# Performance work log

Measured on AMD Instinct MI355X. Metric: run time of the kernel, lower is better.

The kernel has to match this reference:

```python
import jax, jax.numpy as jnp
import numpy as np

V, F, H, R = 10000, 768, 768, 49
B, T = 128, 32


def setup_inputs() -> dict:
    key = jax.random.key(0)
    ks = jax.random.split(key, 12)
    s = lambda *sh: 1.0 / np.sqrt(sh[-1])
    return {
        "features": jax.random.normal(ks[0], (B, R, F), jnp.float32),
        "captions": jax.random.randint(ks[1], (B, T), 0, V),
        "emb_W": jax.random.normal(ks[2], (V, H), jnp.float32),
        "attn_W": jax.random.normal(ks[3], (H, F + H), jnp.float32) * s(H, F + H),
        "attn_b": jnp.zeros((H,), jnp.float32),
        "attnv_W": jax.random.normal(ks[4], (1, H), jnp.float32) * s(1, H),
        "attnv_b": jnp.zeros((1,), jnp.float32),
        "W_ih": jax.random.normal(ks[5], (4 * H, H + F), jnp.float32) * s(1, H),
        "W_hh": jax.random.normal(ks[6], (4 * H, H), jnp.float32) * s(1, H),
        "b_ih": jnp.zeros((4 * H,), jnp.float32),
        "b_hh": jnp.zeros((4 * H,), jnp.float32),
        "fc_W": jax.random.normal(ks[7], (V, H), jnp.float32) * s(V, H),
        "fc_b": jnp.zeros((V,), jnp.float32),
    }


def reference(features, captions, emb_W, attn_W, attn_b, attnv_W, attnv_b,
              W_ih, W_hh, b_ih, b_hh, fc_W, fc_b):
    # initial hidden state (hidden_state=None branch)
    h0 = jnp.tanh(features.mean(axis=1))           # [B,H]
    c0 = jnp.zeros_like(h0)                        # [B,H]
    emb = emb_W[captions]                          # [B,T,H]

    # split attn_linear weight into feature/hidden parts; feature projection is
    # time-invariant so compute once outside the scan.
    Wf, Wh = attn_W[:, :F], attn_W[:, F:]
    feat_proj = jnp.einsum('brf,hf->brh', features, Wf)   # [B,R,H]
    v = attnv_W[0]                                 # [H]
    bias = b_ih + b_hh                             # [4H]

    def step(carry, emb_t):
        h, c = carry
        attn_hidden = jnp.tanh(feat_proj + (h @ Wh.T)[:, None, :] + attn_b)  # [B,R,H]
        scores = attn_hidden @ v + attnv_b[0]      # [B,R]
        alpha = jax.nn.softmax(scores, axis=1)
        context = jnp.einsum('br,brf->bf', alpha, features)  # [B,F]
        x = jnp.concatenate([emb_t, context], axis=1)        # [B,H+F]
        gates = x @ W_ih.T + h @ W_hh.T + bias     # [B,4H]
        i, f, g, o = jnp.split(gates, 4, axis=1)
        c_new = jax.nn.sigmoid(f) * c + jax.nn.sigmoid(i) * jnp.tanh(g)
        h_new = jax.nn.sigmoid(o) * jnp.tanh(c_new)
        out_t = h_new @ fc_W.T + fc_b              # [B,V] (dropout = identity, eval)
        return (h_new, c_new), out_t

    (h, c), outs = jax.lax.scan(step, (h0, c0), jnp.swapaxes(emb, 0, 1))
    outputs = jnp.swapaxes(outs, 0, 1)             # [B,T,V]
    return outputs, (h, c)
```

## Files before the change

kernel.cpp:

```cpp
#include <hip/hip_runtime.h>


typedef _Float16 f16x8 __attribute__((ext_vector_type(8)));
typedef _Float16 f16x4 __attribute__((ext_vector_type(4)));
typedef float f32x4 __attribute__((ext_vector_type(4)));

#define NB 128
#define NT 32
#define NV 10000
#define NH 768
#define NR 49
#define OUT_ELEMS 40960000

__device__ __forceinline__ float fast_tanh(float x) {
  x = fminf(9.f, fmaxf(-9.f, x));
  float e = __expf(2.f * x);
  return (e - 1.f) / (e + 1.f);
}
__device__ __forceinline__ float sigm(float x) { return 1.f / (1.f + __expf(-x)); }

__device__ __forceinline__ void gld16(const void* g, void* l) {
  __builtin_amdgcn_global_load_lds((const __attribute__((address_space(1))) void*)g,
                                   (__attribute__((address_space(3))) void*)l, 16, 0, 0);
}

template <int KSTEPS, int KSPLIT>
__global__ __launch_bounds__(256) void gemm64(
    const _Float16* __restrict__ A, const _Float16* __restrict__ Bt,
    float* __restrict__ C, int N) {
  constexpr int BK = 64;
  __shared__ __attribute__((aligned(16))) _Float16 sAB[128 * BK];
  _Float16* sA = sAB;
  _Float16* sB = sAB + 64 * BK;
  const int tid = threadIdx.x;
  const int m0 = blockIdx.x * 64, n0 = blockIdx.y * 64;
  const int z = blockIdx.z;
  A += (size_t)z * KSPLIT;
  Bt += (size_t)z * KSPLIT;
  C += (size_t)z * 128 * N;

  const int wid = tid >> 6, lane = tid & 63;
  const int wr = wid >> 1, wc = wid & 1;
  const int lr = lane & 15, lk = (lane >> 4) * 8;

  f32x4 acc[2][2] = {};

  for (int kt = 0; kt < KSTEPS; ++kt) {
    const int kbase = kt * BK;
#pragma unroll
    for (int i = 0; i < 2; i++) {
      int idx = tid + i * 256;
      int row = idx >> 3, seg = idx & 7;
      gld16(A + (size_t)(m0 + row) * NH + kbase + seg * 8, sA + idx * 8);
      gld16(Bt + (size_t)(n0 + row) * NH + kbase + seg * 8, sB + idx * 8);
    }
    __syncthreads();
#pragma unroll
    for (int kk = 0; kk < 2; ++kk) {
      f16x8 af[2], bf[2];
#pragma unroll
      for (int m = 0; m < 2; m++)
        af[m] = *(const f16x8*)&sA[(wr * 32 + m * 16 + lr) * BK + kk * 32 + lk];
#pragma unroll
      for (int n = 0; n < 2; n++)
        bf[n] = *(const f16x8*)&sB[(wc * 32 + n * 16 + lr) * BK + kk * 32 + lk];
#pragma unroll
      for (int m = 0; m < 2; m++)
#pragma unroll
        for (int n = 0; n < 2; n++)
          acc[m][n] = __builtin_amdgcn_mfma_f32_16x16x32_f16(af[m], bf[n], acc[m][n], 0, 0, 0);
    }
    __syncthreads();
  }

  const int rowb = (lane >> 4) * 4;
#pragma unroll
  for (int m = 0; m < 2; m++) {
    int gm = m0 + wr * 32 + m * 16 + rowb;
#pragma unroll
    for (int n = 0; n < 2; n++) {
      int gn = n0 + wc * 32 + n * 16 + lr;
#pragma unroll
      for (int j = 0; j < 4; j++) C[(size_t)(gm + j) * N + gn] = acc[m][n][j];
    }
  }
}

__global__ __launch_bounds__(256) void gemm_g2m(
    const _Float16* __restrict__ ctx16, const _Float16* __restrict__ Wc,
    const _Float16* __restrict__ h16, const _Float16* __restrict__ Whh,
    float* __restrict__ C) {
  constexpr int BK = 64;
  __shared__ __attribute__((aligned(16))) _Float16 sAB[128 * BK];
  _Float16* sA = sAB;
  _Float16* sB = sAB + 64 * BK;
  const int tid = threadIdx.x;
  const int m0 = blockIdx.x * 64, n0 = blockIdx.y * 64;
  const int z = blockIdx.z;
  const _Float16* A = (z >> 1) ? h16 : ctx16;
  const _Float16* Bt = (z >> 1) ? Whh : Wc;
  A += (size_t)(z & 1) * 384;
  Bt += (size_t)(z & 1) * 384;
  C += (size_t)z * 128 * 3072;

  const int wid = tid >> 6, lane = tid & 63;
  const int wr = wid >> 1, wc = wid & 1;
  const int lr = lane & 15, lk = (lane >> 4) * 8;

  f32x4 acc[2][2] = {};

  for (int kt = 0; kt < 6; ++kt) {
    const int kbase = kt * BK;
#pragma unroll
    for (int i = 0; i < 2; i++) {
      int idx = tid + i * 256;
      int row = idx >> 3, seg = idx & 7;
      gld16(A + (size_t)(m0 + row) * NH + kbase + seg * 8, sA + idx * 8);
      gld16(Bt + (size_t)(n0 + row) * NH + kbase + seg * 8, sB + idx * 8);
    }
    __syncthreads();
#pragma unroll
    for (int kk = 0; kk < 2; ++kk) {
      f16x8 af[2], bf[2];
#pragma unroll
      for (int m = 0; m < 2; m++)
        af[m] = *(const f16x8*)&sA[(wr * 32 + m * 16 + lr) * BK + kk * 32 + lk];
#pragma unroll
      for (int n = 0; n < 2; n++)
        bf[n] = *(const f16x8*)&sB[(wc * 32 + n * 16 + lr) * BK + kk * 32 + lk];
#pragma unroll
      for (int m = 0; m < 2; m++)
#pragma unroll
        for (int n = 0; n < 2; n++)
          acc[m][n] = __builtin_amdgcn_mfma_f32_16x16x32_f16(af[m], bf[n], acc[m][n], 0, 0, 0);
    }
    __syncthreads();
  }

  const int rowb = (lane >> 4) * 4;
#pragma unroll
  for (int m = 0; m < 2; m++) {
    int gm = m0 + wr * 32 + m * 16 + rowb;
#pragma unroll
    for (int n = 0; n < 2; n++) {
      int gn = n0 + wc * 32 + n * 16 + lr;
#pragma unroll
      for (int j = 0; j < 4; j++) C[(size_t)(gm + j) * 3072 + gn] = acc[m][n][j];
    }
  }
}

__global__ __launch_bounds__(256) void gemm_phA(
    const _Float16* __restrict__ feat16, const _Float16* __restrict__ Wf16,
    const float* __restrict__ attn_b, _Float16* __restrict__ fp16,
    const _Float16* __restrict__ emb16, const _Float16* __restrict__ We16,
    _Float16* __restrict__ Gemb16) {
  constexpr int BK = 64;
  __shared__ __attribute__((aligned(16))) _Float16 sAB[256 * BK];
  _Float16* sA = sAB;
  _Float16* sB = sAB + 128 * BK;
  const int blk = blockIdx.x, tid = threadIdx.x;
  const bool isFP = blk < 294;
  const int bx = isFP ? (blk % 49) : ((blk - 294) % 32);
  const int by = isFP ? (blk / 49) : ((blk - 294) / 32);
  const _Float16* A = isFP ? feat16 : emb16;
  const _Float16* Bt = isFP ? Wf16 : We16;
  const int m0 = bx * 128, n0 = by * 128;

  const int wid = tid >> 6, lane = tid & 63;
  const int wr = wid >> 1, wc = wid & 1;
  const int lr = lane & 15, lk = (lane >> 4) * 8;

  f32x4 acc[4][4] = {};

  for (int kt = 0; kt < 12; ++kt) {
    const int kbase = kt * BK;
#pragma unroll
    for (int i = 0; i < 4; i++) {
      int idx = tid + i * 256;
      int row = idx >> 3, seg = idx & 7;
      gld16(A + (size_t)(m0 + row) * NH + kbase + seg * 8, sA + idx * 8);
      gld16(Bt + (size_t)(n0 + row) * NH + kbase + seg * 8, sB + idx * 8);
    }
    __syncthreads();
#pragma unroll
    for (int kk = 0; kk < 2; ++kk) {
      f16x8 af[4], bf[4];
#pragma unroll
      for (int m = 0; m < 4; m++)
        af[m] = *(const f16x8*)&sA[(wr * 64 + m * 16 + lr) * BK + kk * 32 + lk];
#pragma unroll
      for (int n = 0; n < 4; n++)
        bf[n] = *(const f16x8*)&sB[(wc * 64 + n * 16 + lr) * BK + kk * 32 + lk];
#pragma unroll
      for (int m = 0; m < 4; m++)
#pragma unroll
        for (int n = 0; n < 4; n++)
          acc[m][n] = __builtin_amdgcn_mfma_f32_16x16x32_f16(af[m], bf[n], acc[m][n], 0, 0, 0);
    }
    __syncthreads();
  }

  const int rowb = (lane >> 4) * 4;
#pragma unroll
  for (int m = 0; m < 4; m++) {
    int gm = m0 + wr * 64 + m * 16 + rowb;
#pragma unroll
    for (int n = 0; n < 4; n++) {
      int gn = n0 + wc * 64 + n * 16 + lr;
#pragma unroll
      for (int j = 0; j < 4; j++) {
        if (isFP)
          fp16[(size_t)(gm + j) * NH + gn] = (_Float16)(acc[m][n][j] + attn_b[gn]);
        else
          Gemb16[(size_t)(gm + j) * 3072 + gn] = (_Float16)acc[m][n][j];
      }
    }
  }
}

__global__ __launch_bounds__(256) void gemm_fc(
    const _Float16* __restrict__ A, const _Float16* __restrict__ Bt,
    float* __restrict__ out, const float* __restrict__ bias, int N) {
  constexpr int BK = 64;
  __shared__ __attribute__((aligned(16))) _Float16 sAB[256 * BK];
  _Float16* sA = sAB;
  _Float16* sB = sAB + 128 * BK;
  const int tid = threadIdx.x;
  const int m0 = blockIdx.x * 128, n0 = blockIdx.y * 128;
  const int wid = tid >> 6, lane = tid & 63;
  const int wr = wid >> 1, wc = wid & 1;
  const int lr = lane & 15, lk = (lane >> 4) * 8;

  f32x4 acc[4][4] = {};

  for (int kt = 0; kt < 12; ++kt) {
    const int kbase = kt * BK;
#pragma unroll
    for (int i = 0; i < 4; i++) {
      int idx = tid + i * 256;
      int row = idx >> 3, seg = idx & 7;
      gld16(A + (size_t)(m0 + row) * NH + kbase + seg * 8, sA + idx * 8);
      int gr = n0 + row;
      if (gr >= N) gr = N - 1;
      gld16(Bt + (size_t)gr * NH + kbase + seg * 8, sB + idx * 8);
    }
    __syncthreads();
#pragma unroll
    for (int kk = 0; kk < 2; ++kk) {
      f16x8 af[4], bf[4];
#pragma unroll
      for (int m = 0; m < 4; m++)
        af[m] = *(const f16x8*)&sA[(wr * 64 + m * 16 + lr) * BK + kk * 32 + lk];
#pragma unroll
      for (int n = 0; n < 4; n++)
        bf[n] = *(const f16x8*)&sB[(wc * 64 + n * 16 + lr) * BK + kk * 32 + lk];
#pragma unroll
      for (int m = 0; m < 4; m++)
#pragma unroll
        for (int n = 0; n < 4; n++)
          acc[m][n] = __builtin_amdgcn_mfma_f32_16x16x32_f16(af[m], bf[n], acc[m][n], 0, 0, 0);
    }
    __syncthreads();
  }

  const int rowb = (lane >> 4) * 4;
  float* sC = (float*)sAB;
#pragma unroll
  for (int h = 0; h < 2; h++) {
    if (wr == h) {
#pragma unroll
      for (int m = 0; m < 4; m++)
#pragma unroll
        for (int n = 0; n < 4; n++)
#pragma unroll
          for (int j = 0; j < 4; j++)
            sC[(m * 16 + rowb + j) * 128 + wc * 64 + n * 16 + lr] = acc[m][n][j];
    }
    __syncthreads();
#pragma unroll
    for (int i = 0; i < 8; i++) {
      int lrow = (tid >> 5) + i * 8;
      int col = (tid & 31) * 4;
      int gn = n0 + col;
      if (gn < N) {
        int r = m0 + h * 64 + lrow;
        int tt = r >> 7, b = r & 127;
        f32x4 val = *(f32x4*)&sC[lrow * 128 + col];
        f32x4 bb = *(const f32x4*)&bias[gn];
        val += bb;
        *(f32x4*)&out[((size_t)(b * NT + tt)) * NV + gn] = val;
      }
    }
    __syncthreads();
  }
}

__global__ __launch_bounds__(256) void k_scores(
    const _Float16* __restrict__ fp, const float* __restrict__ g1a,
    const float* __restrict__ v, float* __restrict__ sc) {
  int wid = threadIdx.x >> 6, lane = threadIdx.x & 63;
  int p = blockIdx.x * 4 + wid;
  int b = p / NR;
  const _Float16* fpr = fp + (size_t)p * NH;
  const float* hw0 = g1a + (size_t)b * NH;
  const float* hw1 = g1a + (size_t)NB * NH + (size_t)b * NH;
  const float* hw2 = g1a + (size_t)2 * NB * NH + (size_t)b * NH;
  float s = 0.f;
#pragma unroll
  for (int it = 0; it < 3; it++) {
    int h = it * 256 + lane * 4;
    f16x4 fv = *(const f16x4*)(fpr + h);
    f32x4 a0 = *(const f32x4*)(hw0 + h);
    f32x4 a1 = *(const f32x4*)(hw1 + h);
    f32x4 a2 = *(const f32x4*)(hw2 + h);
    f32x4 vv = *(const f32x4*)(v + h);
#pragma unroll
    for (int j = 0; j < 4; j++) s += fast_tanh((float)fv[j] + a0[j] + a1[j] + a2[j]) * vv[j];
  }
#pragma unroll
  for (int off = 32; off; off >>= 1) s += __shfl_down(s, off);
  if (lane == 0) sc[p] = s;
}

__global__ __launch_bounds__(256) void k_ctx(const float* __restrict__ sc,
                                             const _Float16* __restrict__ feat16,
                                             _Float16* __restrict__ ctx16) {
  __shared__ float al[64];
  int b = blockIdx.x, tid = threadIdx.x;
  if (tid < 64) {
    float s = (tid < NR) ? sc[b * NR + tid] : -1e30f;
    float m = s;
#pragma unroll
    for (int off = 32; off; off >>= 1) m = fmaxf(m, __shfl_xor(m, off));
    float e = (tid < NR) ? __expf(s - m) : 0.f;
    float su = e;
#pragma unroll
    for (int off = 32; off; off >>= 1) su += __shfl_xor(su, off);
    al[tid] = e / su;
  }
  __syncthreads();
  int f = blockIdx.y * 256 + tid;
  const _Float16* fb = feat16 + (size_t)b * NR * NH + f;
  float acc = 0.f;
#pragma unroll
  for (int r = 0; r < NR; r++) acc += al[r] * (float)fb[(size_t)r * NH];
  ctx16[(size_t)b * NH + f] = (_Float16)acc;
}

__global__ void k_lstm2(const _Float16* __restrict__ ge_t, const float* __restrict__ gbuf,
                        const float* __restrict__ b_ih, const float* __restrict__ b_hh,
                        float* __restrict__ h, float* __restrict__ c,
                        _Float16* __restrict__ h16, _Float16* __restrict__ Hall_t) {
  int b = blockIdx.x;
  int hh = blockIdx.y * 256 + threadIdx.x;
  const _Float16* ge = ge_t + (size_t)b * 3072;
  const float* p0 = gbuf + (size_t)b * 3072;
  const float* p1 = p0 + (size_t)NB * 3072;
  const float* p2 = p1 + (size_t)NB * 3072;
  const float* p3 = p2 + (size_t)NB * 3072;
  float gi = (float)ge[hh] + p0[hh] + p1[hh] + p2[hh] + p3[hh] + b_ih[hh] + b_hh[hh];
  float gf = (float)ge[768 + hh] + p0[768 + hh] + p1[768 + hh] + p2[768 + hh] + p3[768 + hh] +
             b_ih[768 + hh] + b_hh[768 + hh];
  float gg = (float)ge[1536 + hh] + p0[1536 + hh] + p1[1536 + hh] + p2[1536 + hh] +
             p3[1536 + hh] + b_ih[1536 + hh] + b_hh[1536 + hh];
  float go = (float)ge[2304 + hh] + p0[2304 + hh] + p1[2304 + hh] + p2[2304 + hh] +
             p3[2304 + hh] + b_ih[2304 + hh] + b_hh[2304 + hh];
  float i_ = sigm(gi), f_ = sigm(gf), g_ = fast_tanh(gg), o_ = sigm(go);
  float cn = f_ * c[b * NH + hh] + i_ * g_;
  float hn = o_ * fast_tanh(cn);
  c[b * NH + hh] = cn;
  h[b * NH + hh] = hn;
  h16[(size_t)b * NH + hh] = (_Float16)hn;
  Hall_t[(size_t)b * NH + hh] = (_Float16)hn;
}

__global__ void k_prep(const float* __restrict__ features, const float* __restrict__ attn_W,
                       const float* __restrict__ W_ih, const float* __restrict__ W_hh,
                       const int* __restrict__ captions, const float* __restrict__ emb_W,
                       _Float16* __restrict__ feat16, _Float16* __restrict__ Wf16,
                       _Float16* __restrict__ Wh16, _Float16* __restrict__ Whh16,
                       _Float16* __restrict__ We, _Float16* __restrict__ Wc,
                       _Float16* __restrict__ emb16, float* __restrict__ h,
                       float* __restrict__ c, _Float16* __restrict__ h16) {
  const int blk = blockIdx.x, tid = threadIdx.x;
  if (blk < 18816) {
    int i = blk * 256 + tid;
    feat16[i] = (_Float16)features[i];
  } else if (blk < 21120) {
    int q = (blk - 18816) * 256 + tid;
    int j = q / NH, k = q - j * NH;
    Wf16[q] = (_Float16)attn_W[(size_t)j * 1536 + k];
  } else if (blk < 23424) {
    int q = (blk - 21120) * 256 + tid;
    int j = q / NH, k = q - j * NH;
    Wh16[q] = (_Float16)attn_W[(size_t)j * 1536 + 768 + k];
  } else if (blk < 32640) {
    int q = (blk - 23424) * 256 + tid;
    Whh16[q] = (_Float16)W_hh[q];
  } else if (blk < 41856) {
    int q = (blk - 32640) * 256 + tid;
    int j = q / NH, k = q - j * NH;
    We[q] = (_Float16)W_ih[(size_t)j * 1536 + k];
  } else if (blk < 51072) {
    int q = (blk - 41856) * 256 + tid;
    int j = q / NH, k = q - j * NH;
    Wc[q] = (_Float16)W_ih[(size_t)j * 1536 + 768 + k];
  } else if (blk < 63360) {
    int q = (blk - 51072) * 256 + tid;
    int row = q / NH, k = q - row * NH;
    int t = row >> 7, b = row & 127;
    int tok = captions[b * NT + t];
    emb16[q] = (_Float16)emb_W[(size_t)tok * NH + k];
  } else {
    int q = blk - 63360;
    int b = q / 3;
    int f = (q - b * 3) * 256 + tid;
    float s = 0.f;
#pragma unroll 7
    for (int r = 0; r < NR; r++) s += features[((size_t)(b * NR + r)) * NH + f];
    float h0 = tanhf(s * (1.f / 49.f));
    h[b * NH + f] = h0;
    c[b * NH + f] = 0.f;
    h16[(size_t)b * NH + f] = (_Float16)h0;
  }
}

__global__ void k_f32_to_f16(const float* __restrict__ src, _Float16* __restrict__ dst, int n) {
  int i = blockIdx.x * 256 + threadIdx.x;
  if (i < n) dst[i] = (_Float16)src[i];
}

__global__ void k_tail(const float* __restrict__ h, const float* __restrict__ c,
                       float* __restrict__ out) {
  int i = blockIdx.x * 256 + threadIdx.x;
  out[OUT_ELEMS + i] = h[i];
  out[OUT_ELEMS + NB * NH + i] = c[i];
}

extern "C" void kernel_launch(void* const* d_in, const int* in_sizes, int n_in,
                              void* d_out, int out_size, void* d_ws, size_t ws_size,
                              hipStream_t stream) {
  const float* features = (const float*)d_in[0];
  const int* captions = (const int*)d_in[1];
  const float* emb_W = (const float*)d_in[2];
  const float* attn_W = (const float*)d_in[3];
  const float* attn_b = (const float*)d_in[4];
  const float* attnv_W = (const float*)d_in[5];
  const float* W_ih = (const float*)d_in[7];
  const float* W_hh = (const float*)d_in[8];
  const float* b_ih = (const float*)d_in[9];
  const float* b_hh = (const float*)d_in[10];
  const float* fc_W = (const float*)d_in[11];
  const float* fc_b = (const float*)d_in[12];
  float* out = (float*)d_out;

  char* p = (char*)d_ws;
  _Float16* Gemb16 = (_Float16*)p;  p += 25165824;
  _Float16* fcW16 = Gemb16;
  _Float16* emb16 = (_Float16*)p;   p += 6291456;
  _Float16* feat16 = (_Float16*)p;  p += 9633792;
  _Float16* fp16 = (_Float16*)p;    p += 9633792;
  _Float16* Wf16 = (_Float16*)p;    p += 1179648;
  _Float16* Wh16 = (_Float16*)p;    p += 1179648;
  _Float16* Whh16 = (_Float16*)p;   p += 4718592;
  _Float16* We16 = (_Float16*)p;    p += 4718592;
  _Float16* Wc16 = (_Float16*)p;    p += 4718592;
  _Float16* H_all = (_Float16*)p;   p += 6291456;
  float* g1a = (float*)p;           p += 1179648;
  float* gbuf = (float*)p;          p += 6291456;
  float* scores = (float*)p;        p += 25088;
  _Float16* ctx16 = (_Float16*)p;   p += 196608;
  _Float16* h16 = (_Float16*)p;     p += 196608;
  float* hbuf = (float*)p;          p += 393216;
  float* cbuf = (float*)p;          p += 393216;

  k_prep<<<dim3(63744), 256, 0, stream>>>(features, attn_W, W_ih, W_hh, captions, emb_W,
                                          feat16, Wf16, Wh16, Whh16, We16, Wc16, emb16,
                                          hbuf, cbuf, h16);
  gemm_phA<<<dim3(1062), 256, 0, stream>>>(feat16, Wf16, attn_b, fp16, emb16, We16, Gemb16);

  for (int t = 0; t < NT; t++) {
    if (t > 0)
      k_lstm2<<<dim3(128, 3), 256, 0, stream>>>(
          Gemb16 + (size_t)(t - 1) * NB * 3072, gbuf, b_ih, b_hh, hbuf, cbuf, h16,
          H_all + (size_t)(t - 1) * NB * NH);
    gemm64<4, 256><<<dim3(2, 12, 3), 256, 0, stream>>>(h16, Wh16, g1a, NH);
    k_scores<<<dim3(1568), 256, 0, stream>>>(fp16, g1a, attnv_W, scores);
    k_ctx<<<dim3(128, 3), 256, 0, stream>>>(scores, feat16, ctx16);
    gemm_g2m<<<dim3(2, 48, 4), 256, 0, stream>>>(ctx16, Wc16, h16, Whh16, gbuf);
  }
  k_lstm2<<<dim3(128, 3), 256, 0, stream>>>(
      Gemb16 + (size_t)(NT - 1) * NB * 3072, gbuf, b_ih, b_hh, hbuf, cbuf, h16,
      H_all + (size_t)(NT - 1) * NB * NH);

  k_f32_to_f16<<<dim3(30000), 256, 0, stream>>>(fc_W, fcW16, 7680000);
  gemm_fc<<<dim3(32, 79), 256, 0, stream>>>(H_all, fcW16, out, fc_b, NV);
  k_tail<<<dim3(384), 256, 0, stream>>>(hbuf, cbuf, out);
}
```

Baseline: 1.023 ms.

## Fuse LSTM cell update into gate GEMM via last-block atomic counter

Interleaves the i/f/g/o rows of the LSTM weight matrices and biases so that each 64-column GEMM tile holds all four gates for 16 hidden units. The gate GEMM then finishes the LSTM cell update itself: whichever of the four split-K blocks arrives last, as counted by an atomic counter, sums the partials and writes c, h and the fp16 hidden state straight into H_all. This removes the separate LSTM kernel launch per step and the extra h16 copy, at the cost of threadfences, atomics and a serialized epilogue in one block per tile.

After: 2.530 ms. +147.4%, slower.

```diff
diff --git a/kernel.cpp b/kernel.cpp
--- a/kernel.cpp
+++ b/kernel.cpp
@@ -86,10 +86,13 @@
   }
 }
 
-__global__ __launch_bounds__(256) void gemm_g2m(
-    const _Float16* __restrict__ ctx16, const _Float16* __restrict__ Wc,
-    const _Float16* __restrict__ h16, const _Float16* __restrict__ Whh,
-    float* __restrict__ C) {
+__global__ __launch_bounds__(256) void g2m_lstm(
+    const _Float16* __restrict__ ctx16, const _Float16* __restrict__ Wc_int,
+    const _Float16* __restrict__ hprev, const _Float16* __restrict__ Whh_int,
+    float* __restrict__ gbuf, const _Float16* __restrict__ ge_t,
+    const float* __restrict__ bias_int, float* __restrict__ cst,
+    float* __restrict__ hst, _Float16* __restrict__ hnext,
+    unsigned* __restrict__ flags) {
   constexpr int BK = 64;
   __shared__ __attribute__((aligned(16))) _Float16 sAB[128 * BK];
   _Float16* sA = sAB;
@@ -97,11 +100,11 @@
   const int tid = threadIdx.x;
   const int m0 = blockIdx.x * 64, n0 = blockIdx.y * 64;
   const int z = blockIdx.z;
-  const _Float16* A = (z >> 1) ? h16 : ctx16;
-  const _Float16* Bt = (z >> 1) ? Whh : Wc;
+  const _Float16* A = (z >> 1) ? hprev : ctx16;
+  const _Float16* Bt = (z >> 1) ? Whh_int : Wc_int;
   A += (size_t)(z & 1) * 384;
   Bt += (size_t)(z & 1) * 384;
-  C += (size_t)z * 128 * 3072;
+  float* C = gbuf + (size_t)z * NB * 3072;
 
   const int wid = tid >> 6, lane = tid & 63;
   const int wr = wid >> 1, wc = wid & 1;
@@ -147,6 +150,42 @@
 #pragma unroll
       for (int j = 0; j < 4; j++) C[(size_t)(gm + j) * 3072 + gn] = acc[m][n][j];
     }
+  }
+
+  __threadfence();
+  __syncthreads();
+  __shared__ unsigned s_old;
+  if (tid == 0) s_old = atomicAdd(&flags[blockIdx.x * 48 + blockIdx.y], 1u);
+  __syncthreads();
+  if (s_old != 3u) return;
+  __threadfence();
+
+  const int b_l = tid & 63, q = tid >> 6;
+  const int b_g = m0 + b_l;
+  const float* g0 = gbuf + (size_t)b_g * 3072;
+  const float* g1 = g0 + (size_t)NB * 3072;
+  const float* g2 = g1 + (size_t)NB * 3072;
+  const float* g3 = g2 + (size_t)NB * 3072;
+#pragma unroll
+  for (int i = 0; i < 4; i++) {
+    int hh_l = q * 4 + i;
+    int hh_g = (n0 >> 2) + hh_l;
+    int colj = n0 + 4 * hh_l;
+    f32x4 s0 = *(const f32x4*)&g0[colj];
+    f32x4 s1 = *(const f32x4*)&g1[colj];
+    f32x4 s2 = *(const f32x4*)&g2[colj];
+    f32x4 s3 = *(const f32x4*)&g3[colj];
+    f16x4 ge = *(const f16x4*)&ge_t[(size_t)b_g * 3072 + colj];
+    f32x4 bi = *(const f32x4*)&bias_int[colj];
+    float gi = s0[0] + s1[0] + s2[0] + s3[0] + (float)ge[0] + bi[0];
+    float gf = s0[1] + s1[1] + s2[1] + s3[1] + (float)ge[1] + bi[1];
+    float gg = s0[2] + s1[2] + s2[2] + s3[2] + (float)ge[2] + bi[2];
+    float go = s0[3] + s1[3] + s2[3] + s3[3] + (float)ge[3] + bi[3];
+    float cn = sigm(gf) * cst[b_g * NH + hh_g] + sigm(gi) * fast_tanh(gg);
+    float hn = sigm(go) * fast_tanh(cn);
+    cst[b_g * NH + hh_g] = cn;
+    hst[b_g * NH + hh_g] = hn;
+    hnext[(size_t)b_g * NH + hh_g] = (_Float16)hn;
   }
 }
 
@@ -348,41 +387,16 @@
   ctx16[(size_t)b * NH + f] = (_Float16)acc;
 }
 
-__global__ void k_lstm2(const _Float16* __restrict__ ge_t, const float* __restrict__ gbuf,
-                        const float* __restrict__ b_ih, const float* __restrict__ b_hh,
-                        float* __restrict__ h, float* __restrict__ c,
-                        _Float16* __restrict__ h16, _Float16* __restrict__ Hall_t) {
-  int b = blockIdx.x;
-  int hh = blockIdx.y * 256 + threadIdx.x;
-  const _Float16* ge = ge_t + (size_t)b * 3072;
-  const float* p0 = gbuf + (size_t)b * 3072;
-  const float* p1 = p0 + (size_t)NB * 3072;
-  const float* p2 = p1 + (size_t)NB * 3072;
-  const float* p3 = p2 + (size_t)NB * 3072;
-  float gi = (float)ge[hh] + p0[hh] + p1[hh] + p2[hh] + p3[hh] + b_ih[hh] + b_hh[hh];
-  float gf = (float)ge[768 + hh] + p0[768 + hh] + p1[768 + hh] + p2[768 + hh] + p3[768 + hh] +
-             b_ih[768 + hh] + b_hh[768 + hh];
-  float gg = (float)ge[1536 + hh] + p0[1536 + hh] + p1[1536 + hh] + p2[1536 + hh] +
-             p3[1536 + hh] + b_ih[1536 + hh] + b_hh[1536 + hh];
-  float go = (float)ge[2304 + hh] + p0[2304 + hh] + p1[2304 + hh] + p2[2304 + hh] +
-             p3[2304 + hh] + b_ih[2304 + hh] + b_hh[2304 + hh];
-  float i_ = sigm(gi), f_ = sigm(gf), g_ = fast_tanh(gg), o_ = sigm(go);
-  float cn = f_ * c[b * NH + hh] + i_ * g_;
-  float hn = o_ * fast_tanh(cn);
-  c[b * NH + hh] = cn;
-  h[b * NH + hh] = hn;
-  h16[(size_t)b * NH + hh] = (_Float16)hn;
-  Hall_t[(size_t)b * NH + hh] = (_Float16)hn;
-}
-
 __global__ void k_prep(const float* __restrict__ features, const float* __restrict__ attn_W,
                        const float* __restrict__ W_ih, const float* __restrict__ W_hh,
                        const int* __restrict__ captions, const float* __restrict__ emb_W,
+                       const float* __restrict__ b_ih, const float* __restrict__ b_hh,
                        _Float16* __restrict__ feat16, _Float16* __restrict__ Wf16,
-                       _Float16* __restrict__ Wh16, _Float16* __restrict__ Whh16,
-                       _Float16* __restrict__ We, _Float16* __restrict__ Wc,
+                       _Float16* __restrict__ Wh16, _Float16* __restrict__ Whh_int,
+                       _Float16* __restrict__ We_int, _Float16* __restrict__ Wc_int,
                        _Float16* __restrict__ emb16, float* __restrict__ h,
-                       float* __restrict__ c, _Float16* __restrict__ h16) {
+                       float* __restrict__ c, _Float16* __restrict__ h0_16,
+                       unsigned* __restrict__ flags, float* __restrict__ bias_int) {
   const int blk = blockIdx.x, tid = threadIdx.x;
   if (blk < 18816) {
     int i = blk * 256 + tid;
@@ -397,22 +411,26 @@
     Wh16[q] = (_Float16)attn_W[(size_t)j * 1536 + 768 + k];
   } else if (blk < 32640) {
     int q = (blk - 23424) * 256 + tid;
-    Whh16[q] = (_Float16)W_hh[q];
+    int jp = q / NH, k = q - jp * NH;
+    int src = (jp & 3) * NH + (jp >> 2);
+    Whh_int[q] = (_Float16)W_hh[(size_t)src * NH + k];
   } else if (blk < 41856) {
     int q = (blk - 32640) * 256 + tid;
-    int j = q / NH, k = q - j * NH;
-    We[q] = (_Float16)W_ih[(size_t)j * 1536 + k];
+    int jp = q / NH, k = q - jp * NH;
+    int src = (jp & 3) * NH + (jp >> 2);
+    We_int[q] = (_Float16)W_ih[(size_t)src * 1536 + k];
   } else if (blk < 51072) {
     int q = (blk - 41856) * 256 + tid;
-    int j = q / NH, k = q - j * NH;
-    Wc[q] = (_Float16)W_ih[(size_t)j * 1536 + 768 + k];
+    int jp = q / NH, k = q - jp * NH;
+    int src = (jp & 3) * NH + (jp >> 2);
+    Wc_int[q] = (_Float16)W_ih[(size_t)src * 1536 + 768 + k];
   } else if (blk < 63360) {
     int q = (blk - 51072) * 256 + tid;
     int row = q / NH, k = q - row * NH;
     int t = row >> 7, b = row & 127;
     int tok = captions[b * NT + t];
     emb16[q] = (_Float16)emb_W[(size_t)tok * NH + k];
-  } else {
+  } else if (blk < 63744) {
     int q = blk - 63360;
     int b = q / 3;
     int f = (q - b * 3) * 256 + tid;
@@ -422,7 +440,13 @@
     float h0 = tanhf(s * (1.f / 49.f));
     h[b * NH + f] = h0;
     c[b * NH + f] = 0.f;
-    h16[(size_t)b * NH + f] = (_Float16)h0;
+    h0_16[(size_t)b * NH + f] = (_Float16)h0;
+  } else if (blk < 63756) {
+    flags[(blk - 63744) * 256 + tid] = 0u;
+  } else {
+    int q = (blk - 63756) * 256 + tid;
+    int src = (q & 3) * NH + (q >> 2);
+    bias_int[q] = b_ih[src] + b_hh[src];
   }
 }
 
@@ -463,36 +487,35 @@
   _Float16* fp16 = (_Float16*)p;    p += 9633792;
   _Float16* Wf16 = (_Float16*)p;    p += 1179648;
   _Float16* Wh16 = (_Float16*)p;    p += 1179648;
-  _Float16* Whh16 = (_Float16*)p;   p += 4718592;
-  _Float16* We16 = (_Float16*)p;    p += 4718592;
-  _Float16* Wc16 = (_Float16*)p;    p += 4718592;
+  _Float16* Whh_int = (_Float16*)p; p += 4718592;
+  _Float16* We_int = (_Float16*)p;  p += 4718592;
+  _Float16* Wc_int = (_Float16*)p;  p += 4718592;
   _Float16* H_all = (_Float16*)p;   p += 6291456;
+  _Float16* h0_16 = (_Float16*)p;   p += 196608;
   float* g1a = (float*)p;           p += 1179648;
   float* gbuf = (float*)p;          p += 6291456;
   float* scores = (float*)p;        p += 25088;
   _Float16* ctx16 = (_Float16*)p;   p += 196608;
-  _Float16* h16 = (_Float16*)p;     p += 196608;
   float* hbuf = (float*)p;          p += 393216;
   float* cbuf = (float*)p;          p += 393216;
-
-  k_prep<<<dim3(63744), 256, 0, stream>>>(features, attn_W, W_ih, W_hh, captions, emb_W,
-                                          feat16, Wf16, Wh16, Whh16, We16, Wc16, emb16,
-                                          hbuf, cbuf, h16);
-  gemm_phA<<<dim3(1062), 256, 0, stream>>>(feat16, Wf16, attn_b, fp16, emb16, We16, Gemb16);
+  float* bias_int = (float*)p;      p += 12288;
+  unsigned* flags = (unsigned*)p;   p += 12288;
+
+  k_prep<<<dim3(63768), 256, 0, stream>>>(features, attn_W, W_ih, W_hh, captions, emb_W,
+                                          b_ih, b_hh, feat16, Wf16, Wh16, Whh_int,
+                                          We_int, Wc_int, emb16, hbuf, cbuf, h0_16,
+                                          flags, bias_int);
+  gemm_phA<<<dim3(1062), 256, 0, stream>>>(feat16, Wf16, attn_b, fp16, emb16, We_int, Gemb16);
 
   for (int t = 0; t < NT; t++) {
-    if (t > 0)
-      k_lstm2<<<dim3(128, 3), 256, 0, stream>>>(
-          Gemb16 + (size_t)(t - 1) * NB * 3072, gbuf, b_ih, b_hh, hbuf, cbuf, h16,
-          H_all + (size_t)(t - 1) * NB * NH);
-    gemm64<4, 256><<<dim3(2, 12, 3), 256, 0, stream>>>(h16, Wh16, g1a, NH);
+    const _Float16* hin = (t == 0) ? h0_16 : H_all + (size_t)(t - 1) * NB * NH;
+    gemm64<4, 256><<<dim3(2, 12, 3), 256, 0, stream>>>(hin, Wh16, g1a, NH);
     k_scores<<<dim3(1568), 256, 0, stream>>>(fp16, g1a, attnv_W, scores);
     k_ctx<<<dim3(128, 3), 256, 0, stream>>>(scores, feat16, ctx16);
-    gemm_g2m<<<dim3(2, 48, 4), 256, 0, stream>>>(ctx16, Wc16, h16, Whh16, gbuf);
-  }
-  k_lstm2<<<dim3(128, 3), 256, 0, stream>>>(
-      Gemb16 + (size_t)(NT - 1) * NB * 3072, gbuf, b_ih, b_hh, hbuf, cbuf, h16,
-      H_all + (size_t)(NT - 1) * NB * NH);
+    g2m_lstm<<<dim3(2, 48, 4), 256, 0, stream>>>(
+        ctx16, Wc_int, hin, Whh_int, gbuf, Gemb16 + (size_t)t * NB * 3072, bias_int,
+        cbuf, hbuf, H_all + (size_t)t * NB * NH, flags + (size_t)t * 96);
+  }
 
   k_f32_to_f16<<<dim3(30000), 256, 0, stream>>>(fc_W, fcW16, 7680000);
   gemm_fc<<<dim3(32, 79), 256, 0, stream>>>(H_all, fcW16, out, fc_b, NV);
```
